# Performance work log

Hardware: AMD Instinct MI355X
Metric: run time of the kernel (lower is better)

The kernel has to match this reference:

```python
import jax, jax.numpy as jnp
import numpy as np

TEMP = 0.07
EPS = 1e-12  # matches torch F.normalize default eps


def _l2norm(x):
    n = jnp.sqrt(jnp.sum(x * x, axis=-1, keepdims=True))
    return x / jnp.maximum(n, EPS)


def setup_inputs() -> dict:
    key = jax.random.key(0)
    kq, kk = jax.random.split(key)
    N, D = 16384, 256
    q = jax.random.normal(kq, (N, D), dtype=jnp.float32)
    k = jax.random.normal(kk, (N, D), dtype=jnp.float32)
    return {"q": q, "k": k}


def reference(q, k):
    qn = _l2norm(q)
    kn = _l2norm(k)
    logits = (qn @ kn.T) / TEMP            # [N, N]
    # cross-entropy with labels = arange(N): mean over rows of (logsumexp - diag)
    lse = jax.nn.logsumexp(logits, axis=-1)  # [N]
    diag = jnp.diagonal(logits)              # [N]
    return jnp.mean(lse - diag)
```

## Files before the change

### kernel.cpp

```cpp
#include <hip/hip_runtime.h>
#include <hip/hip_bf16.h>
#include <cstdint>
#include <cstddef>

#define NROWS 16384
#define DDIM  256
#define SPLITS 16
#define NTILES 256
#define TILES_PER (NTILES / SPLITS)

typedef __attribute__((ext_vector_type(4))) float f32x4;
typedef __attribute__((ext_vector_type(4))) float fl4;
typedef __attribute__((ext_vector_type(4))) int   i32x4;
typedef __attribute__((ext_vector_type(8))) int   i32x8;

constexpr float SCALE_EXP2 = 20.609929155556627f;
constexpr float LN2F       = 0.69314718055994531f;
constexpr float INV_T      = 14.285714285714286f;

__device__ inline void gload_lds16(const void* g, void* l) {
  __builtin_amdgcn_global_load_lds(
      (const __attribute__((address_space(1))) void*)g,
      (__attribute__((address_space(3))) void*)l, 16, 0, 0);
}

__global__ __launch_bounds__(256) void norm_kernel(
    const float* __restrict__ q, const float* __restrict__ k,
    unsigned char* __restrict__ qn, unsigned char* __restrict__ kn,
    float* __restrict__ diag, float* __restrict__ rowsum,
    float* __restrict__ out)
{
  const int wave = threadIdx.x >> 6, lane = threadIdx.x & 63;
  const int row = blockIdx.x * 4 + wave;
  const size_t off = (size_t)row * DDIM + lane * 4;

  fl4 vq = *(const fl4*)(q + off);
  fl4 vk = *(const fl4*)(k + off);
  float ssq = vq.x * vq.x + vq.y * vq.y + vq.z * vq.z + vq.w * vq.w;
  float ssk = vk.x * vk.x + vk.y * vk.y + vk.z * vk.z + vk.w * vk.w;
  float dot = vq.x * vk.x + vq.y * vk.y + vq.z * vk.z + vq.w * vk.w;
#pragma unroll
  for (int m = 1; m < 64; m <<= 1) {
    ssq += __shfl_xor(ssq, m, 64);
    ssk += __shfl_xor(ssk, m, 64);
    dot += __shfl_xor(dot, m, 64);
  }
  float rq = 1.0f / fmaxf(sqrtf(ssq), 1e-12f);
  float rk = 1.0f / fmaxf(sqrtf(ssk), 1e-12f);

  float sq = rq * SCALE_EXP2;
  int pq = __builtin_amdgcn_cvt_pk_fp8_f32(vq.x * sq, vq.y * sq, 0, false);
  pq     = __builtin_amdgcn_cvt_pk_fp8_f32(vq.z * sq, vq.w * sq, pq, true);
  *(int*)(qn + off) = pq;
  int pk = __builtin_amdgcn_cvt_pk_fp8_f32(vk.x * rk, vk.y * rk, 0, false);
  pk     = __builtin_amdgcn_cvt_pk_fp8_f32(vk.z * rk, vk.w * rk, pk, true);
  *(int*)(kn + off) = pk;

  if (lane == 0) {
    diag[row]   = dot * rq * rk * INV_T;
    rowsum[row] = 0.0f;
    if (row == 0) out[0] = 0.0f;
  }
}

__global__ __launch_bounds__(256) void lse_kernel(
    const unsigned char* __restrict__ qn, const unsigned char* __restrict__ kn,
    float* __restrict__ rowsum)
{
  __shared__ __attribute__((aligned(16))) unsigned char Bs[2][64 * DDIM];

  const int tid  = threadIdx.x;
  const int wave = tid >> 6, lane = tid & 63;
  const int l15  = lane & 15, quad = lane >> 4;
  const int wr   = wave >> 1, wc = wave & 1;
  const int split = blockIdx.x % SPLITS;
  const int rb    = blockIdx.x / SPLITS;
  const int wrow  = rb * 128 + wr * 64;
  const int t0 = split * TILES_PER;
  const int t1 = t0 + TILES_PER;

  const int Ln = tid >> 4, Ljj = tid & 15;
  const int Lj = Ljj ^ Ln;
  const size_t src_off = (size_t)Ln * DDIM + (size_t)Lj * 16;

  i32x8 A00, A01, A10, A11, A20, A21, A30, A31;
  {
    const unsigned char* ap0 = qn + (size_t)(wrow      + l15) * DDIM + quad * 32;
    const unsigned char* ap1 = qn + (size_t)(wrow + 16 + l15) * DDIM + quad * 32;
    const unsigned char* ap2 = qn + (size_t)(wrow + 32 + l15) * DDIM + quad * 32;
    const unsigned char* ap3 = qn + (size_t)(wrow + 48 + l15) * DDIM + quad * 32;
    A00 = *(const i32x8*)(ap0);  A01 = *(const i32x8*)(ap0 + 128);
    A10 = *(const i32x8*)(ap1);  A11 = *(const i32x8*)(ap1 + 128);
    A20 = *(const i32x8*)(ap2);  A21 = *(const i32x8*)(ap2 + 128);
    A30 = *(const i32x8*)(ap3);  A31 = *(const i32x8*)(ap3 + 128);
  }

  const int rowoff = l15 * DDIM;
  const int c0  = quad * 2;
  const int o00 = rowoff + (((c0    ) ^ l15) * 16);
  const int o01 = rowoff + (((c0 + 1) ^ l15) * 16);
  const int o10 = rowoff + (((c0 + 8) ^ l15) * 16);
  const int o11 = rowoff + (((c0 + 9) ^ l15) * 16);
  const int cb0 = wc * 8192;

  f32x4 sums0 = {0.f,0.f,0.f,0.f}, sums1 = {0.f,0.f,0.f,0.f};
  f32x4 sums2 = {0.f,0.f,0.f,0.f}, sums3 = {0.f,0.f,0.f,0.f};
  f32x4 accE0, accE1, accE2, accE3, accO0, accO1, accO2, accO3;
  accO0 = (f32x4){-1e30f, -1e30f, -1e30f, -1e30f};
  accO1 = accO0; accO2 = accO0; accO3 = accO0;

  {
    const unsigned char* kbase = kn + (size_t)t0 * (64 * DDIM) + src_off;
#pragma unroll
    for (int i = 0; i < 4; ++i)
      gload_lds16(kbase + i * 4096, (void*)(Bs[0] + tid * 16 + i * 4096));
  }

#define EPI1(Pv, Sv) do {                                                     \
    f32x4 e_;                                                                 \
    e_[0] = __builtin_amdgcn_exp2f(Pv[0]);                                    \
    e_[1] = __builtin_amdgcn_exp2f(Pv[1]);                                    \
    e_[2] = __builtin_amdgcn_exp2f(Pv[2]);                                    \
    e_[3] = __builtin_amdgcn_exp2f(Pv[3]);                                    \
    Sv += e_;                                                                 \
  } while (0)

#define EPI(P) do {                                                           \
    EPI1(P##0, sums0); EPI1(P##1, sums1);                                     \
    EPI1(P##2, sums2); EPI1(P##3, sums3);                                     \
  } while (0)

#define CS_STEP(C, P, BOFF) do {                                              \
    i32x4 lo0_ = *(const i32x4*)(bb + (BOFF) + o00);                          \
    i32x4 hi0_ = *(const i32x4*)(bb + (BOFF) + o01);                          \
    i32x4 lo1_ = *(const i32x4*)(bb + (BOFF) + o10);                          \
    i32x4 hi1_ = *(const i32x4*)(bb + (BOFF) + o11);                          \
    EPI(P);                \
    i32x8 b0_ = {lo0_.x, lo0_.y, lo0_.z, lo0_.w, hi0_.x, hi0_.y, hi0_.z, hi0_.w}; \
    i32x8 b1_ = {lo1_.x, lo1_.y, lo1_.z, lo1_.w, hi1_.x, hi1_.y, hi1_.z, hi1_.w}; \
    __builtin_amdgcn_s_setprio(1);                                            \
    C##0 = __builtin_amdgcn_mfma_scale_f32_16x16x128_f8f6f4(                  \
        A00, b0_, (f32x4){0.f, 0.f, 0.f, 0.f}, 0, 0, 0, 127, 0, 127);         \
    C##1 = __builtin_amdgcn_mfma_scale_f32_16x16x128_f8f6f4(                  \
        A10, b0_, (f32x4){0.f, 0.f, 0.f, 0.f}, 0, 0, 0, 127, 0, 127);         \
    C##2 = __builtin_amdgcn_mfma_scale_f32_16x16x128_f8f6f4(                  \
        A20, b0_, (f32x4){0.f, 0.f, 0.f, 0.f}, 0, 0, 0, 127, 0, 127);         \
    C##3 = __builtin_amdgcn_mfma_scale_f32_16x16x128_f8f6f4(                  \
        A30, b0_, (f32x4){0.f, 0.f, 0.f, 0.f}, 0, 0, 0, 127, 0, 127);         \
    C##0 = __builtin_amdgcn_mfma_scale_f32_16x16x128_f8f6f4(                  \
        A01, b1_, C##0, 0, 0, 0, 127, 0, 127);                                \
    C##1 = __builtin_amdgcn_mfma_scale_f32_16x16x128_f8f6f4(                  \
        A11, b1_, C##1, 0, 0, 0, 127, 0, 127);                                \
    C##2 = __builtin_amdgcn_mfma_scale_f32_16x16x128_f8f6f4(                  \
        A21, b1_, C##2, 0, 0, 0, 127, 0, 127);                                \
    C##3 = __builtin_amdgcn_mfma_scale_f32_16x16x128_f8f6f4(                  \
        A31, b1_, C##3, 0, 0, 0, 127, 0, 127);                                \
    __builtin_amdgcn_s_setprio(0);                                            \
  } while (0)

  for (int ct = t0; ct < t1; ++ct) {
    const int cur = (ct - t0) & 1;
    __builtin_amdgcn_s_waitcnt(0x0F70);
    __syncthreads();
    if (ct + 1 < t1) {
      const unsigned char* kbase = kn + (size_t)(ct + 1) * (64 * DDIM) + src_off;
#pragma unroll
      for (int i = 0; i < 4; ++i)
        gload_lds16(kbase + i * 4096, (void*)(Bs[cur ^ 1] + tid * 16 + i * 4096));
    }
    const unsigned char* bb = Bs[cur];
    CS_STEP(accE, accO, cb0);
    CS_STEP(accO, accE, cb0 + 4096);
  }
  EPI(accO);

#undef CS_STEP
#undef EPI
#undef EPI1

#define RED(Sv, SROW) do {                                                    \
    _Pragma("unroll")                                                         \
    for (int r = 0; r < 4; ++r) {                                             \
      float v = Sv[r];                                                        \
      v += __shfl_xor(v, 1, 64);                                              \
      v += __shfl_xor(v, 2, 64);                                              \
      v += __shfl_xor(v, 4, 64);                                              \
      v += __shfl_xor(v, 8, 64);                                              \
      if (l15 == 0) atomicAdd(&rowsum[(SROW) + quad * 4 + r], v);             \
    }                                                                         \
  } while (0)

  RED(sums0, wrow);
  RED(sums1, wrow + 16);
  RED(sums2, wrow + 32);
  RED(sums3, wrow + 48);
#undef RED
}

__global__ void final_kernel(const float* __restrict__ rowsum,
                             const float* __restrict__ diag,
                             float* __restrict__ out)
{
  int row = blockIdx.x * 256 + threadIdx.x;
  float c = __builtin_amdgcn_logf(rowsum[row]) * LN2F - diag[row];
#pragma unroll
  for (int m = 1; m < 64; m <<= 1) c += __shfl_xor(c, m, 64);
  __shared__ float red[4];
  int wave = threadIdx.x >> 6, lane = threadIdx.x & 63;
  if (lane == 0) red[wave] = c;
  __syncthreads();
  if (threadIdx.x == 0) {
    float s = red[0] + red[1] + red[2] + red[3];
    atomicAdd(out, s * (1.0f / NROWS));
  }
}

extern "C" void kernel_launch(void* const* d_in, const int* in_sizes, int n_in,
                              void* d_out, int out_size, void* d_ws, size_t ws_size,
                              hipStream_t stream)
{
  const float* q = (const float*)d_in[0];
  const float* k = (const float*)d_in[1];
  float* out = (float*)d_out;

  char* ws = (char*)d_ws;
  unsigned char* qn = (unsigned char*)ws;
  unsigned char* kn = (unsigned char*)(ws + (4u << 20));
  float* diag   = (float*)(ws + (8u << 20));
  float* rowsum = (float*)(ws + (8u << 20) + (64u << 10));

  norm_kernel <<<NROWS / 4, 256, 0, stream>>>(q, k, qn, kn, diag, rowsum, out);
  lse_kernel  <<<(NROWS / 128) * SPLITS, 256, 0, stream>>>(qn, kn, rowsum);
  final_kernel<<<NROWS / 256, 256, 0, stream>>>(rowsum, diag, out);
}
```

Before: 148.3 us.

## Load K fragments directly from global into registers, dropping LDS staging

Removes the shared-memory double buffer and the per-tile __syncthreads; each wave now reads its K-tile fragments straight from global memory into registers with a one-step software prefetch. The wave-column split becomes a contiguous 512-column range per wave instead of interleaved halves of shared 64-row tiles. This drops the barrier and LDS read traffic, but each wave pair now fetches K independently (duplicate global/L2 reads) and load latency is hidden only by a single-stage register prefetch.

```diff
diff --git a/kernel.cpp b/kernel.cpp
--- a/kernel.cpp
+++ b/kernel.cpp
@@ -6,8 +6,6 @@
 #define NROWS 16384
 #define DDIM  256
 #define SPLITS 16
-#define NTILES 256
-#define TILES_PER (NTILES / SPLITS)
 
 typedef __attribute__((ext_vector_type(4))) float f32x4;
 typedef __attribute__((ext_vector_type(4))) float fl4;
@@ -17,12 +15,6 @@
 constexpr float SCALE_EXP2 = 20.609929155556627f;
 constexpr float LN2F       = 0.69314718055994531f;
 constexpr float INV_T      = 14.285714285714286f;
-
-__device__ inline void gload_lds16(const void* g, void* l) {
-  __builtin_amdgcn_global_load_lds(
-      (const __attribute__((address_space(1))) void*)g,
-      (__attribute__((address_space(3))) void*)l, 16, 0, 0);
-}
 
 __global__ __launch_bounds__(256) void norm_kernel(
     const float* __restrict__ q, const float* __restrict__ k,
@@ -67,8 +59,6 @@
     const unsigned char* __restrict__ qn, const unsigned char* __restrict__ kn,
     float* __restrict__ rowsum)
 {
-  __shared__ __attribute__((aligned(16))) unsigned char Bs[2][64 * DDIM];
-
   const int tid  = threadIdx.x;
   const int wave = tid >> 6, lane = tid & 63;
   const int l15  = lane & 15, quad = lane >> 4;
@@ -76,12 +66,7 @@
   const int split = blockIdx.x % SPLITS;
   const int rb    = blockIdx.x / SPLITS;
   const int wrow  = rb * 128 + wr * 64;
-  const int t0 = split * TILES_PER;
-  const int t1 = t0 + TILES_PER;
-
-  const int Ln = tid >> 4, Ljj = tid & 15;
-  const int Lj = Ljj ^ Ln;
-  const size_t src_off = (size_t)Ln * DDIM + (size_t)Lj * 16;
+  const int col0  = split * (NROWS / SPLITS) + wc * 512;
 
   i32x8 A00, A01, A10, A11, A20, A21, A30, A31;
   {
@@ -95,13 +80,7 @@
     A30 = *(const i32x8*)(ap3);  A31 = *(const i32x8*)(ap3 + 128);
   }
 
-  const int rowoff = l15 * DDIM;
-  const int c0  = quad * 2;
-  const int o00 = rowoff + (((c0    ) ^ l15) * 16);
-  const int o01 = rowoff + (((c0 + 1) ^ l15) * 16);
-  const int o10 = rowoff + (((c0 + 8) ^ l15) * 16);
-  const int o11 = rowoff + (((c0 + 9) ^ l15) * 16);
-  const int cb0 = wc * 8192;
+  const unsigned char* kb = kn + (size_t)(col0 + l15) * DDIM + quad * 32;
 
   f32x4 sums0 = {0.f,0.f,0.f,0.f}, sums1 = {0.f,0.f,0.f,0.f};
   f32x4 sums2 = {0.f,0.f,0.f,0.f}, sums3 = {0.f,0.f,0.f,0.f};
@@ -109,12 +88,8 @@
   accO0 = (f32x4){-1e30f, -1e30f, -1e30f, -1e30f};
   accO1 = accO0; accO2 = accO0; accO3 = accO0;
 
-  {
-    const unsigned char* kbase = kn + (size_t)t0 * (64 * DDIM) + src_off;
-#pragma unroll
-    for (int i = 0; i < 4; ++i)
-      gload_lds16(kbase + i * 4096, (void*)(Bs[0] + tid * 16 + i * 4096));
-  }
+  i32x8 b0c = *(const i32x8*)(kb);
+  i32x8 b1c = *(const i32x8*)(kb + 128);
 
 #define EPI1(Pv, Sv) do {                                                     \
     f32x4 e_;                                                                 \
@@ -130,51 +105,49 @@
     EPI1(P##2, sums2); EPI1(P##3, sums3);                                     \
   } while (0)
 
-#define CS_STEP(C, P, BOFF) do {                                              \
-    i32x4 lo0_ = *(const i32x4*)(bb + (BOFF) + o00);                          \
-    i32x4 hi0_ = *(const i32x4*)(bb + (BOFF) + o01);                          \
-    i32x4 lo1_ = *(const i32x4*)(bb + (BOFF) + o10);                          \
-    i32x4 hi1_ = *(const i32x4*)(bb + (BOFF) + o11);                          \
-    EPI(P);                \
-    i32x8 b0_ = {lo0_.x, lo0_.y, lo0_.z, lo0_.w, hi0_.x, hi0_.y, hi0_.z, hi0_.w}; \
-    i32x8 b1_ = {lo1_.x, lo1_.y, lo1_.z, lo1_.w, hi1_.x, hi1_.y, hi1_.z, hi1_.w}; \
+#define MFMA8(C, B0, B1) do {                                                 \
     __builtin_amdgcn_s_setprio(1);                                            \
     C##0 = __builtin_amdgcn_mfma_scale_f32_16x16x128_f8f6f4(                  \
-        A00, b0_, (f32x4){0.f, 0.f, 0.f, 0.f}, 0, 0, 0, 127, 0, 127);         \
+        A00, B0, (f32x4){0.f, 0.f, 0.f, 0.f}, 0, 0, 0, 127, 0, 127);          \
     C##1 = __builtin_amdgcn_mfma_scale_f32_16x16x128_f8f6f4(                  \
-        A10, b0_, (f32x4){0.f, 0.f, 0.f, 0.f}, 0, 0, 0, 127, 0, 127);         \
+        A10, B0, (f32x4){0.f, 0.f, 0.f, 0.f}, 0, 0, 0, 127, 0, 127);          \
     C##2 = __builtin_amdgcn_mfma_scale_f32_16x16x128_f8f6f4(                  \
-        A20, b0_, (f32x4){0.f, 0.f, 0.f, 0.f}, 0, 0, 0, 127, 0, 127);         \
+        A20, B0, (f32x4){0.f, 0.f, 0.f, 0.f}, 0, 0, 0, 127, 0, 127);          \
     C##3 = __builtin_amdgcn_mfma_scale_f32_16x16x128_f8f6f4(                  \
-        A30, b0_, (f32x4){0.f, 0.f, 0.f, 0.f}, 0, 0, 0, 127, 0, 127);         \
+        A30, B0, (f32x4){0.f, 0.f, 0.f, 0.f}, 0, 0, 0, 127, 0, 127);          \
     C##0 = __builtin_amdgcn_mfma_scale_f32_16x16x128_f8f6f4(                  \
-        A01, b1_, C##0, 0, 0, 0, 127, 0, 127);                                \
+        A01, B1, C##0, 0, 0, 0, 127, 0, 127);                                 \
     C##1 = __builtin_amdgcn_mfma_scale_f32_16x16x128_f8f6f4(                  \
-        A11, b1_, C##1, 0, 0, 0, 127, 0, 127);                                \
+        A11, B1, C##1, 0, 0, 0, 127, 0, 127);                                 \
     C##2 = __builtin_amdgcn_mfma_scale_f32_16x16x128_f8f6f4(                  \
-        A21, b1_, C##2, 0, 0, 0, 127, 0, 127);                                \
+        A21, B1, C##2, 0, 0, 0, 127, 0, 127);                                 \
     C##3 = __builtin_amdgcn_mfma_scale_f32_16x16x128_f8f6f4(                  \
-        A31, b1_, C##3, 0, 0, 0, 127, 0, 127);                                \
+        A31, B1, C##3, 0, 0, 0, 127, 0, 127);                                 \
     __builtin_amdgcn_s_setprio(0);                                            \
   } while (0)
 
-  for (int ct = t0; ct < t1; ++ct) {
-    const int cur = (ct - t0) & 1;
-    __builtin_amdgcn_s_waitcnt(0x0F70);
-    __syncthreads();
-    if (ct + 1 < t1) {
-      const unsigned char* kbase = kn + (size_t)(ct + 1) * (64 * DDIM) + src_off;
-#pragma unroll
-      for (int i = 0; i < 4; ++i)
-        gload_lds16(kbase + i * 4096, (void*)(Bs[cur ^ 1] + tid * 16 + i * 4096));
-    }
-    const unsigned char* bb = Bs[cur];
-    CS_STEP(accE, accO, cb0);
-    CS_STEP(accO, accE, cb0 + 4096);
+  for (int it = 0; it < 15; ++it) {
+    i32x8 b0n = *(const i32x8*)(kb + 4096);
+    i32x8 b1n = *(const i32x8*)(kb + 4096 + 128);
+    EPI(accO);
+    MFMA8(accE, b0c, b1c);
+    b0c = *(const i32x8*)(kb + 8192);
+    b1c = *(const i32x8*)(kb + 8192 + 128);
+    EPI(accE);
+    MFMA8(accO, b0n, b1n);
+    kb += 8192;
+  }
+  {
+    i32x8 b0n = *(const i32x8*)(kb + 4096);
+    i32x8 b1n = *(const i32x8*)(kb + 4096 + 128);
+    EPI(accO);
+    MFMA8(accE, b0c, b1c);
+    EPI(accE);
+    MFMA8(accO, b0n, b1n);
   }
   EPI(accO);
 
-#undef CS_STEP
+#undef MFMA8
 #undef EPI
 #undef EPI1
 
```

After: 207.8 us. 40.1% more time.
